# Optimization experiments

Measured on AMD Instinct MI355X. Metric: run time of the kernel, lower is better.

The kernel has to match this reference:

```python
import jax, jax.numpy as jnp
import numpy as np

B, N, D = 2, 2048, 1024
H, DH = 16, 64
DEPTH = 4
FF = 4
EPS = 1e-3  # keras LayerNormalization default epsilon
SCALE = DH ** -0.5


def setup_inputs() -> dict:
    key = jax.random.key(0)
    ks = jax.random.split(key, 8)
    s = 0.02
    inner = H * DH
    return {
        "x": jax.random.normal(ks[0], (B, N, D), jnp.float32),
        "mask": jnp.ones((B, N), jnp.bool_),
        "ln1_g": jnp.ones((DEPTH, D), jnp.float32),
        "ln1_b": jnp.zeros((DEPTH, D), jnp.float32),
        "Wqkv": jax.random.normal(ks[1], (DEPTH, D, 3 * inner), jnp.float32) * s,
        "Wout": jax.random.normal(ks[2], (DEPTH, inner, D), jnp.float32) * s,
        "bout": jnp.zeros((DEPTH, D), jnp.float32),
        "ln2_g": jnp.ones((DEPTH, D), jnp.float32),
        "ln2_b": jnp.zeros((DEPTH, D), jnp.float32),
        "W1": jax.random.normal(ks[3], (DEPTH, D, 2 * FF * D), jnp.float32) * s,
        "b1": jnp.zeros((DEPTH, 2 * FF * D), jnp.float32),
        "W2": jax.random.normal(ks[4], (DEPTH, FF * D, D), jnp.float32) * s,
        "b2": jnp.zeros((DEPTH, D), jnp.float32),
    }


def _layernorm(x, g, b):
    mu = jnp.mean(x, axis=-1, keepdims=True)
    var = jnp.mean(jnp.square(x - mu), axis=-1, keepdims=True)
    return (x - mu) * jax.lax.rsqrt(var + EPS) * g + b


def _attention(x, mask, Wqkv, Wout, bout):
    b, n, _ = x.shape
    qkv = x @ Wqkv  # [b, n, 3*h*dh]
    q, k, v = jnp.split(qkv, 3, axis=-1)
    split_heads = lambda t: t.reshape(b, n, H, DH).transpose(0, 2, 1, 3)  # b h n d
    q, k, v = split_heads(q), split_heads(k), split_heads(v)
    dots = jnp.einsum("bhid,bhjd->bhij", q, k) * SCALE
    neg = -jnp.finfo(dots.dtype).max
    # padding mask: keep (i valid) & (j valid)
    pm = mask[:, None, :, None] & mask[:, None, None, :]
    dots = jnp.where(pm, dots, neg)
    # causal mask: strict upper triangle masked out (triu with k=1)
    causal = jnp.triu(jnp.ones((n, n), jnp.bool_), k=1)
    dots = jnp.where(causal, neg, dots)
    attn = jax.nn.softmax(dots, axis=-1)
    out = jnp.einsum("bhij,bhjd->bhid", attn, v)
    out = out.transpose(0, 2, 1, 3).reshape(b, n, H * DH)
    return out @ Wout + bout


def _feedforward(x, W1, b1, W2, b2):
    h = x @ W1 + b1
    a, gates = jnp.split(h, 2, axis=-1)
    h = a * jax.nn.gelu(gates, approximate=False)  # GEGLU, tf.nn.gelu exact
    return h @ W2 + b2


def reference(x, mask, ln1_g, ln1_b, Wqkv, Wout, bout, ln2_g, ln2_b, W1, b1, W2, b2):
    for l in range(DEPTH):
        x = x + _attention(_layernorm(x, ln1_g[l], ln1_b[l]), mask, Wqkv[l], Wout[l], bout[l])
        x = x + _feedforward(_layernorm(x, ln2_g[l], ln2_b[l]), W1[l], b1[l], W2[l], b2[l])
    return x
```

## Files before the change

kernel.cpp:

```cpp
#include <hip/hip_runtime.h>


typedef float f32x4 __attribute__((ext_vector_type(4)));
typedef __bf16 bf16x8 __attribute__((ext_vector_type(8)));
typedef unsigned short u16;
typedef unsigned int u32;

#define SCALE2 0.18033688011112042f
#define LN_EPS 1e-3f
#define DEFER_THR 8.0f

__device__ __forceinline__ float fexp2(float x) { return __builtin_amdgcn_exp2f(x); }

__device__ __forceinline__ u16 f2bf(float f) {
  u32 u = __float_as_uint(f);
  u += 0x7fffu + ((u >> 16) & 1u);
  return (u16)(u >> 16);
}

__device__ __forceinline__ void stage16(void* lds_wave_base, const void* gsrc) {
  __builtin_amdgcn_global_load_lds((__attribute__((address_space(1))) void*)gsrc,
                                   (__attribute__((address_space(3))) void*)lds_wave_base,
                                   16, 0, 0);
}

__global__ void wtrans_kernel(const float* __restrict__ W, u16* __restrict__ WT,
                              int K, int N, int permMode) {
  __shared__ float tile[32][33];
  const int n0 = blockIdx.x * 32, k0 = blockIdx.y * 32;
  const float* Wl = W + (size_t)blockIdx.z * K * N;
  u16* WTl = WT + (size_t)blockIdx.z * K * N;
  const int tx = threadIdx.x, ty = threadIdx.y;
#pragma unroll
  for (int i = 0; i < 4; ++i)
    tile[ty + i * 8][tx] = Wl[(size_t)(k0 + ty + i * 8) * N + n0 + tx];
  __syncthreads();
#pragma unroll
  for (int i = 0; i < 4; ++i) {
    const int n = n0 + ty + i * 8;
    int orow;
    if (permMode) {
      orow = (n < 4096) ? (((n >> 4) << 5) + (n & 15))
                        : ((((n - 4096) >> 4) << 5) + 16 + (n & 15));
    } else {
      orow = n;
    }
    WTl[(size_t)orow * K + k0 + tx] = f2bf(tile[tx][ty + i * 8]);
  }
}

__global__ __launch_bounds__(256, 4)
void ln_kernel(const float* __restrict__ x, const float* __restrict__ g,
               const float* __restrict__ b, u16* __restrict__ y) {
  const int row = blockIdx.x, tid = threadIdx.x;
  const float4 v = ((const float4*)(x + (size_t)row * 1024))[tid];
  float s = v.x + v.y + v.z + v.w;
  float s2 = v.x * v.x + v.y * v.y + v.z * v.z + v.w * v.w;
#pragma unroll
  for (int off = 32; off > 0; off >>= 1) {
    s += __shfl_down(s, off);
    s2 += __shfl_down(s2, off);
  }
  __shared__ float ps[8];
  __shared__ float stats[2];
  const int wv = tid >> 6, lane = tid & 63;
  if (lane == 0) { ps[wv] = s; ps[wv + 4] = s2; }
  __syncthreads();
  if (tid == 0) {
    const float S = ps[0] + ps[1] + ps[2] + ps[3];
    const float S2 = ps[4] + ps[5] + ps[6] + ps[7];
    const float mu = S * (1.0f / 1024.0f);
    const float var = S2 * (1.0f / 1024.0f) - mu * mu;
    stats[0] = mu;
    stats[1] = rsqrtf(var + LN_EPS);
  }
  __syncthreads();
  const float mu = stats[0], rs = stats[1];
  const float4 gg = ((const float4*)g)[tid];
  const float4 bb = ((const float4*)b)[tid];
  ushort4 ov;
  ov.x = f2bf((v.x - mu) * rs * gg.x + bb.x);
  ov.y = f2bf((v.y - mu) * rs * gg.y + bb.y);
  ov.z = f2bf((v.z - mu) * rs * gg.z + bb.z);
  ov.w = f2bf((v.w - mu) * rs * gg.w + bb.w);
  ((ushort4*)(y + (size_t)row * 1024))[tid] = ov;
}

template <int EPI, int BM, int BN, int WM, int WN>
__global__ __launch_bounds__(WM * WN * 64, 2)
void gemm4(const u16* __restrict__ A, const u16* __restrict__ B,
           float* __restrict__ resid, const float* __restrict__ bias,
           u16* __restrict__ out, u16* __restrict__ vt, int M, int N, int K) {
  constexpr int NTHR = WM * WN * 64;
  constexpr int MT = BM / WM / 16;
  constexpr int NT = BN / WN / 16;
  __shared__ __align__(16) u16 lds[2][(BM + BN) * 64];

  const int tid = threadIdx.x;
  const int wv = tid >> 6, lane = tid & 63;
  const int lr = lane & 15, lg = lane >> 4;
  const int wmi = wv / WN, wni = wv % WN;
  const int RB0 = wmi * (BM / WM), CB0 = wni * (BN / WN);

  const int nwg = (int)(gridDim.x * gridDim.y);
  int id = (int)(blockIdx.y * gridDim.x + blockIdx.x);
  id = (id & 7) * (nwg >> 3) + (id >> 3);
  const int m0 = (id / (int)gridDim.x) * BM, n0 = (id % (int)gridDim.x) * BN;

  auto stage = [&](int bsel, int k0) {
    u16* dstA = &lds[bsel][0];
    u16* dstB = &lds[bsel][BM * 64];
#pragma unroll
    for (int rnd = 0; rnd < (BM * 128) / (NTHR * 16); ++rnd) {
      const int base = rnd * (NTHR * 16) + wv * 1024;
      const int off = base + lane * 16;
      const int row = off >> 7;
      const int k2 = (off & 127) ^ ((row & 7) << 4);
      stage16((char*)dstA + base, A + (size_t)(m0 + row) * K + k0 + (k2 >> 1));
    }
#pragma unroll
    for (int rnd = 0; rnd < (BN * 128) / (NTHR * 16); ++rnd) {
      const int base = rnd * (NTHR * 16) + wv * 1024;
      const int off = base + lane * 16;
      const int row = off >> 7;
      const int k2 = (off & 127) ^ ((row & 7) << 4);
      stage16((char*)dstB + base, B + (size_t)(n0 + row) * K + k0 + (k2 >> 1));
    }
  };

  f32x4 acc[MT][NT] = {};
  bf16x8 afr0[MT], bfr0[NT], afr1[MT], bfr1[NT];

  auto rd = [&](int bsel, int ks, bf16x8 (&af)[MT], bf16x8 (&bf)[NT]) {
    const char* As = (const char*)&lds[bsel][0];
    const char* Bs = (const char*)&lds[bsel][BM * 64];
#pragma unroll
    for (int mt = 0; mt < MT; ++mt) {
      const int row = RB0 + mt * 16 + lr;
      af[mt] = *(const bf16x8*)(As + row * 128 + ((ks * 64 + lg * 16) ^ ((lr & 7) << 4)));
    }
#pragma unroll
    for (int nt = 0; nt < NT; ++nt) {
      const int row = CB0 + nt * 16 + lr;
      bf[nt] = *(const bf16x8*)(Bs + row * 128 + ((ks * 64 + lg * 16) ^ ((lr & 7) << 4)));
    }
  };

  const int nT = K >> 6;
  stage(0, 0);
  stage(1, 64);
  asm volatile("s_waitcnt vmcnt(8)\n\ts_barrier" ::: "memory");
  rd(0, 0, afr0, bfr0);
  __builtin_amdgcn_sched_barrier(0);

  for (int t = 0; t < nT; ++t) {
    const int c = t & 1;
    rd(c, 1, afr1, bfr1);
    __builtin_amdgcn_sched_barrier(0);
    __builtin_amdgcn_s_setprio(1);
#pragma unroll
    for (int mt = 0; mt < MT; ++mt)
#pragma unroll
      for (int nt = 0; nt < NT; ++nt)
        acc[mt][nt] = __builtin_amdgcn_mfma_f32_16x16x32_bf16(
            afr0[mt], bfr0[nt], acc[mt][nt], 0, 0, 0);
    __builtin_amdgcn_s_setprio(0);
    __builtin_amdgcn_sched_barrier(0);
    asm volatile("s_waitcnt lgkmcnt(0)\n\ts_barrier" ::: "memory");
    __builtin_amdgcn_sched_barrier(0);
    if (t + 2 < nT) stage(c, (t + 2) * 64);
    if (t + 1 < nT) {
      if (t + 2 < nT)
        asm volatile("s_waitcnt vmcnt(8)\n\ts_barrier" ::: "memory");
      else
        asm volatile("s_waitcnt vmcnt(0)\n\ts_barrier" ::: "memory");
      rd(c ^ 1, 0, afr0, bfr0);
      __builtin_amdgcn_sched_barrier(0);
    }
    __builtin_amdgcn_s_setprio(1);
#pragma unroll
    for (int mt = 0; mt < MT; ++mt)
#pragma unroll
      for (int nt = 0; nt < NT; ++nt)
        acc[mt][nt] = __builtin_amdgcn_mfma_f32_16x16x32_bf16(
            afr1[mt], bfr1[nt], acc[mt][nt], 0, 0, 0);
    __builtin_amdgcn_s_setprio(0);
  }

  if (EPI == 0) {
#pragma unroll
    for (int mt = 0; mt < MT; ++mt)
#pragma unroll
      for (int nt = 0; nt < NT; ++nt) {
        const int n = n0 + CB0 + nt * 16 + lr;
#pragma unroll
        for (int r = 0; r < 4; ++r) {
          const int m = m0 + RB0 + mt * 16 + lg * 4 + r;
          out[(size_t)m * N + n] = f2bf(acc[mt][nt][r]);
        }
      }
  } else if (EPI == 1) {
    float bs[NT];
#pragma unroll
    for (int nt = 0; nt < NT; ++nt) bs[nt] = bias[n0 + CB0 + nt * 16 + lr];
#pragma unroll
    for (int mt = 0; mt < MT; ++mt)
#pragma unroll
      for (int nt = 0; nt < NT; ++nt) {
        const int n = n0 + CB0 + nt * 16 + lr;
#pragma unroll
        for (int r = 0; r < 4; ++r) {
          const int m = m0 + RB0 + mt * 16 + lg * 4 + r;
          resid[(size_t)m * N + n] += acc[mt][nt][r] + bs[nt];
        }
      }
  } else if (EPI == 2) {
#pragma unroll
    for (int pt = 0; pt < NT / 2; ++pt) {
      const int colA = ((n0 + CB0 + pt * 32) >> 5) * 16 + lr;
      const float ba = bias[colA];
      const float bg = bias[4096 + colA];
#pragma unroll
      for (int mt = 0; mt < MT; ++mt)
#pragma unroll
        for (int r = 0; r < 4; ++r) {
          const int m = m0 + RB0 + mt * 16 + lg * 4 + r;
          const float a = acc[mt][2 * pt][r] + ba;
          const float g = acc[mt][2 * pt + 1][r] + bg;
          const float gl = 0.5f * g * (1.0f + erff(g * 0.70710678118654752f));
          out[(size_t)m * 4096 + colA] = f2bf(a * gl);
        }
    }
  } else {
    if (n0 + CB0 < 2048) {
#pragma unroll
      for (int mt = 0; mt < MT; ++mt)
#pragma unroll
        for (int nt = 0; nt < NT; ++nt) {
          const int n = n0 + CB0 + nt * 16 + lr;
#pragma unroll
          for (int r = 0; r < 4; ++r) {
            const int m = m0 + RB0 + mt * 16 + lg * 4 + r;
            out[(size_t)m * N + n] = f2bf(acc[mt][nt][r]);
          }
        }
    } else {
      const int bidx = m0 >> 11;
      const int tokb = (m0 & 2047) + RB0 + lg * 4;
#pragma unroll
      for (int mt = 0; mt < MT; ++mt)
#pragma unroll
        for (int nt = 0; nt < NT; ++nt) {
          const int n = n0 + CB0 + nt * 16 + lr;
          const int hv = (n - 2048) >> 6;
          const int d = (n - 2048) & 63;
          ushort4 w;
          w.x = f2bf(acc[mt][nt][0]);
          w.y = f2bf(acc[mt][nt][1]);
          w.z = f2bf(acc[mt][nt][2]);
          w.w = f2bf(acc[mt][nt][3]);
          *(ushort4*)(vt + ((size_t)(bidx * 16 + hv) * 64 + d) * 2048 +
                      tokb + mt * 16) = w;
        }
    }
  }
}

__global__ __launch_bounds__(512, 4)
void attn_kernel(const u16* __restrict__ qkv, const u16* __restrict__ Vt,
                 u16* __restrict__ attnout) {
  __shared__ __align__(16) u16 KV[4][2][64 * 64];
  __shared__ __align__(16) u16 Ps[8][16 * 64];

  const int tid = threadIdx.x;
  const int wv = tid >> 6, lane = tid & 63;
  const int lr = lane & 15, lg = lane >> 4;
  const int lin = (int)(blockIdx.y * gridDim.x + blockIdx.x);
  const int xcd = lin & 7, j = lin >> 3;
  const int bh = xcd * 4 + (j >> 4);
  const int pr = j & 15;
  const int b = bh >> 4, h = bh & 15;
  const size_t tokbase = (size_t)b * 2048;
  const int qhi = 31 - pr;
  const int qt = (wv < 4) ? qhi : pr;
  const int ws = wv & 3;
  const int qg = qt * 64 + ws * 16 + lr;

  bf16x8 qf[2];
#pragma unroll
  for (int ks = 0; ks < 2; ++ks)
    qf[ks] = *(const bf16x8*)(qkv + (tokbase + qt * 64 + ws * 16 + lr) * 3072 +
                              h * 64 + ks * 32 + lg * 8);

  f32x4 o[4] = {};
  float m = -1e30f, lp = 0.f;

  const u16* kg_base = qkv + tokbase * 3072 + 1024 + h * 64;
  const u16* vg_base = Vt + (size_t)bh * 64 * 2048;

  const int soff = tid * 16;
  const int srow = soff >> 7;
  const int scol = (soff & 127) ^ ((srow & 7) << 4);
  auto stage = [&](int bsel, int kt2) {
    stage16((char*)&KV[bsel][0][0] + wv * 1024,
            kg_base + (size_t)(kt2 * 64 + srow) * 3072 + (scol >> 1));
    stage16((char*)&KV[bsel][1][0] + wv * 1024,
            vg_base + (size_t)srow * 2048 + kt2 * 64 + (scol >> 1));
  };

  auto compute = [&](int kt) {
    const char* Ks = (const char*)&KV[kt & 3][0][0];
    const char* Vs = (const char*)&KV[kt & 3][1][0];

    f32x4 s[4] = {};
#pragma unroll
    for (int ks = 0; ks < 2; ++ks)
#pragma unroll
      for (int nt = 0; nt < 4; ++nt) {
        const int row = nt * 16 + lr;
        const bf16x8 kf = *(const bf16x8*)(Ks + row * 128 +
                                           ((ks * 64 + lg * 16) ^ ((lr & 7) << 4)));
        s[nt] = __builtin_amdgcn_mfma_f32_16x16x32_bf16(kf, qf[ks], s[nt], 0, 0, 0);
      }

    float pmax = -1e30f;
    const bool diag = (kt == qt);
#pragma unroll
    for (int nt = 0; nt < 4; ++nt)
#pragma unroll
      for (int r = 0; r < 4; ++r) {
        float v = s[nt][r] * SCALE2;
        if (diag) {
          const int kg = kt * 64 + nt * 16 + lg * 4 + r;
          v = (kg <= qg) ? v : -1e30f;
        }
        s[nt][r] = v;
        pmax = fmaxf(pmax, v);
      }

    if (!__all(pmax - m <= DEFER_THR)) {
      float mx = fmaxf(pmax, __shfl_xor(pmax, 16));
      mx = fmaxf(mx, __shfl_xor(mx, 32));
      const float mn = fmaxf(m, mx);
      const float alpha = fexp2(m - mn);
      m = mn;
      lp *= alpha;
#pragma unroll
      for (int r = 0; r < 4; ++r) {
        const float ar = __shfl(alpha, lg * 4 + r);
#pragma unroll
        for (int dt = 0; dt < 4; ++dt) o[dt][r] *= ar;
      }
    }

#pragma unroll
    for (int nt = 0; nt < 4; ++nt) {
      const float p0 = fexp2(s[nt][0] - m), p1 = fexp2(s[nt][1] - m);
      const float p2 = fexp2(s[nt][2] - m), p3 = fexp2(s[nt][3] - m);
      lp += (p0 + p1) + (p2 + p3);
      uint2 w;
      w.x = (u32)f2bf(p0) | ((u32)f2bf(p1) << 16);
      w.y = (u32)f2bf(p2) | ((u32)f2bf(p3) << 16);
      *(uint2*)((char*)&Ps[wv][0] + lr * 128 + ((nt * 32 + lg * 8) ^ ((lr & 7) << 4))) = w;
    }

    bf16x8 pf[2];
#pragma unroll
    for (int ks = 0; ks < 2; ++ks) {
      const int jp = (ks * 4 + lg) ^ (lr & 7);
      pf[ks] = *(const bf16x8*)(&Ps[wv][0] + lr * 64 + jp * 8);
    }
#pragma unroll
    for (int ks = 0; ks < 2; ++ks)
#pragma unroll
      for (int dt = 0; dt < 4; ++dt) {
        const int row = dt * 16 + lr;
        const bf16x8 vf = *(const bf16x8*)(Vs + row * 128 +
                                           ((ks * 64 + lg * 16) ^ ((lr & 7) << 4)));
        o[dt] = __builtin_amdgcn_mfma_f32_16x16x32_bf16(pf[ks], vf, o[dt], 0, 0, 0);
      }
  };

  stage(0, 0); stage(1, 1); stage(2, 2); stage(3, 3);
  asm volatile("s_waitcnt vmcnt(4)\n\ts_barrier" ::: "memory");

  for (int kt = 0; kt <= qhi; kt += 2) {
    if (kt <= qt) compute(kt);
    if (kt + 1 <= qt) compute(kt + 1);
    asm volatile("s_barrier" ::: "memory");
    if (kt + 4 <= qhi) stage((kt + 4) & 3, kt + 4);
    if (kt + 5 <= qhi) stage((kt + 5) & 3, kt + 5);
    if (kt + 2 <= qhi) {
      if (kt + 4 <= qhi)
        asm volatile("s_waitcnt vmcnt(4)\n\ts_barrier" ::: "memory");
      else
        asm volatile("s_waitcnt vmcnt(0)\n\ts_barrier" ::: "memory");
    }
  }

  float lsum = lp + __shfl_xor(lp, 16);
  lsum += __shfl_xor(lsum, 32);
#pragma unroll
  for (int r = 0; r < 4; ++r) {
    const float ld = __shfl(lsum, lg * 4 + r);
    const int tok = qt * 64 + ws * 16 + lg * 4 + r;
#pragma unroll
    for (int dt = 0; dt < 4; ++dt)
      attnout[(tokbase + tok) * 1024 + h * 64 + dt * 16 + lr] = f2bf(o[dt][r] / ld);
  }
}

extern "C" void kernel_launch(void* const* d_in, const int* in_sizes, int n_in,
                              void* d_out, int out_size, void* d_ws, size_t ws_size,
                              hipStream_t stream) {
  (void)in_sizes; (void)n_in; (void)ws_size;
  const float* x_in  = (const float*)d_in[0];
  const float* ln1_g = (const float*)d_in[2];
  const float* ln1_b = (const float*)d_in[3];
  const float* Wqkv  = (const float*)d_in[4];
  const float* Wout  = (const float*)d_in[5];
  const float* bout  = (const float*)d_in[6];
  const float* ln2_g = (const float*)d_in[7];
  const float* ln2_b = (const float*)d_in[8];
  const float* W1    = (const float*)d_in[9];
  const float* b1    = (const float*)d_in[10];
  const float* W2    = (const float*)d_in[11];
  const float* b2    = (const float*)d_in[12];
  float* x = (float*)d_out;

  char* ws = (char*)d_ws;
  size_t off = 0;
  auto alloc = [&](size_t bytes) -> void* {
    void* p = ws + off;
    off += (bytes + 255) & ~(size_t)255;
    return p;
  };
  u16* WqkvT = (u16*)alloc(4ull * 3072 * 1024 * 2);
  u16* WoutT = (u16*)alloc(4ull * 1024 * 1024 * 2);
  u16* W1T   = (u16*)alloc(4ull * 8192 * 1024 * 2);
  u16* W2T   = (u16*)alloc(4ull * 1024 * 4096 * 2);
  u16* y     = (u16*)alloc(4096ull * 1024 * 2);
  u16* qkvb  = (u16*)alloc(4096ull * 3072 * 2);
  u16* Vt    = (u16*)alloc(32ull * 64 * 2048 * 2);
  u16* attn  = (u16*)alloc(4096ull * 1024 * 2);
  u16* ff    = (u16*)alloc(4096ull * 4096 * 2);

  hipMemcpyAsync(x, x_in, (size_t)out_size * 4, hipMemcpyDeviceToDevice, stream);

  const dim3 tb(32, 8);
  wtrans_kernel<<<dim3(3072 / 32, 1024 / 32, 4), tb, 0, stream>>>(Wqkv, WqkvT, 1024, 3072, 0);
  wtrans_kernel<<<dim3(1024 / 32, 1024 / 32, 4), tb, 0, stream>>>(Wout, WoutT, 1024, 1024, 0);
  wtrans_kernel<<<dim3(8192 / 32, 1024 / 32, 4), tb, 0, stream>>>(W1, W1T, 1024, 8192, 1);
  wtrans_kernel<<<dim3(1024 / 32, 4096 / 32, 4), tb, 0, stream>>>(W2, W2T, 4096, 1024, 0);

  for (int l = 0; l < 4; ++l) {
    ln_kernel<<<4096, 256, 0, stream>>>(x, ln1_g + l * 1024, ln1_b + l * 1024, y);
    gemm4<3, 128, 128, 2, 2><<<dim3(3072 / 128, 4096 / 128), 256, 0, stream>>>(
        y, WqkvT + (size_t)l * 3072 * 1024, nullptr, nullptr, qkvb, Vt, 4096, 3072, 1024);
    attn_kernel<<<dim3(16, 32), 512, 0, stream>>>(qkvb, Vt, attn);
    gemm4<1, 128, 128, 2, 2><<<dim3(1024 / 128, 4096 / 128), 256, 0, stream>>>(
        attn, WoutT + (size_t)l * 1024 * 1024, x, bout + l * 1024, nullptr, nullptr,
        4096, 1024, 1024);
    ln_kernel<<<4096, 256, 0, stream>>>(x, ln2_g + l * 1024, ln2_b + l * 1024, y);
    gemm4<2, 256, 256, 2, 4><<<dim3(8192 / 256, 4096 / 256), 512, 0, stream>>>(
        y, W1T + (size_t)l * 8192 * 1024, nullptr, b1 + l * 8192, ff, nullptr,
        4096, 8192, 1024);
    gemm4<1, 128, 128, 2, 2><<<dim3(1024 / 128, 4096 / 128), 256, 0, stream>>>(
        ff, W2T + (size_t)l * 1024 * 4096, x, b2 + l * 1024, nullptr, nullptr,
        4096, 1024, 4096);
  }
}
```

Before: 1.118 ms.

## Replace GEMM template with fixed 128x128 tile, K-step 32 kernel

Replaces the templated GEMM with a fixed 128x128, 4-wave kernel that stages K in 32-wide chunks with a new XOR swizzle, and drops the register double-buffering of LDS fragments. LDS use per block shrinks, so launch bounds rise to 4 blocks per CU for higher occupancy. The FF1 GEMM moves from 256x256 tiles to 128x128 tiles. The trade-off is more barriers per K, less latency hiding from fragment prefetch, and lower reuse for the large GEMM.

After: 1.239 ms. 1.11x slower.

```diff
diff --git a/kernel.cpp b/kernel.cpp
--- a/kernel.cpp
+++ b/kernel.cpp
@@ -86,112 +86,91 @@
   ((ushort4*)(y + (size_t)row * 1024))[tid] = ov;
 }
 
-template <int EPI, int BM, int BN, int WM, int WN>
-__global__ __launch_bounds__(WM * WN * 64, 2)
-void gemm4(const u16* __restrict__ A, const u16* __restrict__ B,
+template <int EPI>
+__global__ __launch_bounds__(256, 4)
+void gemm6(const u16* __restrict__ A, const u16* __restrict__ B,
            float* __restrict__ resid, const float* __restrict__ bias,
            u16* __restrict__ out, u16* __restrict__ vt, int M, int N, int K) {
-  constexpr int NTHR = WM * WN * 64;
-  constexpr int MT = BM / WM / 16;
-  constexpr int NT = BN / WN / 16;
-  __shared__ __align__(16) u16 lds[2][(BM + BN) * 64];
+  __shared__ __align__(16) u16 lds[2][256 * 32];
 
   const int tid = threadIdx.x;
   const int wv = tid >> 6, lane = tid & 63;
   const int lr = lane & 15, lg = lane >> 4;
-  const int wmi = wv / WN, wni = wv % WN;
-  const int RB0 = wmi * (BM / WM), CB0 = wni * (BN / WN);
+  const int wmi = wv >> 1, wni = wv & 1;
+  const int RB0 = wmi * 64, CB0 = wni * 64;
 
   const int nwg = (int)(gridDim.x * gridDim.y);
   int id = (int)(blockIdx.y * gridDim.x + blockIdx.x);
   id = (id & 7) * (nwg >> 3) + (id >> 3);
-  const int m0 = (id / (int)gridDim.x) * BM, n0 = (id % (int)gridDim.x) * BN;
+  const int m0 = (id / (int)gridDim.x) * 128, n0 = (id % (int)gridDim.x) * 128;
 
   auto stage = [&](int bsel, int k0) {
     u16* dstA = &lds[bsel][0];
-    u16* dstB = &lds[bsel][BM * 64];
-#pragma unroll
-    for (int rnd = 0; rnd < (BM * 128) / (NTHR * 16); ++rnd) {
-      const int base = rnd * (NTHR * 16) + wv * 1024;
+    u16* dstB = &lds[bsel][128 * 32];
+#pragma unroll
+    for (int rnd = 0; rnd < 2; ++rnd) {
+      const int base = rnd * 4096 + wv * 1024;
       const int off = base + lane * 16;
-      const int row = off >> 7;
-      const int k2 = (off & 127) ^ ((row & 7) << 4);
-      stage16((char*)dstA + base, A + (size_t)(m0 + row) * K + k0 + (k2 >> 1));
-    }
-#pragma unroll
-    for (int rnd = 0; rnd < (BN * 128) / (NTHR * 16); ++rnd) {
-      const int base = rnd * (NTHR * 16) + wv * 1024;
+      const int row = off >> 6;
+      const int gslot = ((off >> 4) & 3) ^ ((row >> 1) & 3);
+      stage16((char*)dstA + base, A + (size_t)(m0 + row) * K + k0 + gslot * 8);
+    }
+#pragma unroll
+    for (int rnd = 0; rnd < 2; ++rnd) {
+      const int base = rnd * 4096 + wv * 1024;
       const int off = base + lane * 16;
-      const int row = off >> 7;
-      const int k2 = (off & 127) ^ ((row & 7) << 4);
-      stage16((char*)dstB + base, B + (size_t)(n0 + row) * K + k0 + (k2 >> 1));
+      const int row = off >> 6;
+      const int gslot = ((off >> 4) & 3) ^ ((row >> 1) & 3);
+      stage16((char*)dstB + base, B + (size_t)(n0 + row) * K + k0 + gslot * 8);
     }
   };
 
-  f32x4 acc[MT][NT] = {};
-  bf16x8 afr0[MT], bfr0[NT], afr1[MT], bfr1[NT];
-
-  auto rd = [&](int bsel, int ks, bf16x8 (&af)[MT], bf16x8 (&bf)[NT]) {
-    const char* As = (const char*)&lds[bsel][0];
-    const char* Bs = (const char*)&lds[bsel][BM * 64];
-#pragma unroll
-    for (int mt = 0; mt < MT; ++mt) {
-      const int row = RB0 + mt * 16 + lr;
-      af[mt] = *(const bf16x8*)(As + row * 128 + ((ks * 64 + lg * 16) ^ ((lr & 7) << 4)));
-    }
-#pragma unroll
-    for (int nt = 0; nt < NT; ++nt) {
-      const int row = CB0 + nt * 16 + lr;
-      bf[nt] = *(const bf16x8*)(Bs + row * 128 + ((ks * 64 + lg * 16) ^ ((lr & 7) << 4)));
-    }
-  };
-
-  const int nT = K >> 6;
+  f32x4 acc[4][4] = {};
+  bf16x8 af[4], bf[4];
+
+  const int nT = K >> 5;
   stage(0, 0);
-  stage(1, 64);
-  asm volatile("s_waitcnt vmcnt(8)\n\ts_barrier" ::: "memory");
-  rd(0, 0, afr0, bfr0);
-  __builtin_amdgcn_sched_barrier(0);
+  stage(1, 32);
+  asm volatile("s_waitcnt vmcnt(4)\n\ts_barrier" ::: "memory");
 
   for (int t = 0; t < nT; ++t) {
     const int c = t & 1;
-    rd(c, 1, afr1, bfr1);
-    __builtin_amdgcn_sched_barrier(0);
+    const char* As = (const char*)&lds[c][0];
+    const char* Bs = (const char*)&lds[c][128 * 32];
+#pragma unroll
+    for (int mt = 0; mt < 4; ++mt) {
+      const int row = RB0 + mt * 16 + lr;
+      af[mt] = *(const bf16x8*)(As + row * 64 + ((lg * 16) ^ (((row >> 1) & 3) << 4)));
+    }
+#pragma unroll
+    for (int nt = 0; nt < 4; ++nt) {
+      const int row = CB0 + nt * 16 + lr;
+      bf[nt] = *(const bf16x8*)(Bs + row * 64 + ((lg * 16) ^ (((row >> 1) & 3) << 4)));
+    }
     __builtin_amdgcn_s_setprio(1);
 #pragma unroll
-    for (int mt = 0; mt < MT; ++mt)
-#pragma unroll
-      for (int nt = 0; nt < NT; ++nt)
+    for (int mt = 0; mt < 4; ++mt)
+#pragma unroll
+      for (int nt = 0; nt < 4; ++nt)
         acc[mt][nt] = __builtin_amdgcn_mfma_f32_16x16x32_bf16(
-            afr0[mt], bfr0[nt], acc[mt][nt], 0, 0, 0);
+            af[mt], bf[nt], acc[mt][nt], 0, 0, 0);
     __builtin_amdgcn_s_setprio(0);
-    __builtin_amdgcn_sched_barrier(0);
     asm volatile("s_waitcnt lgkmcnt(0)\n\ts_barrier" ::: "memory");
     __builtin_amdgcn_sched_barrier(0);
-    if (t + 2 < nT) stage(c, (t + 2) * 64);
+    if (t + 2 < nT) stage(c, (t + 2) * 32);
     if (t + 1 < nT) {
       if (t + 2 < nT)
-        asm volatile("s_waitcnt vmcnt(8)\n\ts_barrier" ::: "memory");
+        asm volatile("s_waitcnt vmcnt(4)\n\ts_barrier" ::: "memory");
       else
         asm volatile("s_waitcnt vmcnt(0)\n\ts_barrier" ::: "memory");
-      rd(c ^ 1, 0, afr0, bfr0);
-      __builtin_amdgcn_sched_barrier(0);
-    }
-    __builtin_amdgcn_s_setprio(1);
-#pragma unroll
-    for (int mt = 0; mt < MT; ++mt)
-#pragma unroll
-      for (int nt = 0; nt < NT; ++nt)
-        acc[mt][nt] = __builtin_amdgcn_mfma_f32_16x16x32_bf16(
-            afr1[mt], bfr1[nt], acc[mt][nt], 0, 0, 0);
-    __builtin_amdgcn_s_setprio(0);
+    }
   }
 
   if (EPI == 0) {
 #pragma unroll
-    for (int mt = 0; mt < MT; ++mt)
-#pragma unroll
-      for (int nt = 0; nt < NT; ++nt) {
+    for (int mt = 0; mt < 4; ++mt)
+#pragma unroll
+      for (int nt = 0; nt < 4; ++nt) {
         const int n = n0 + CB0 + nt * 16 + lr;
 #pragma unroll
         for (int r = 0; r < 4; ++r) {
@@ -200,13 +179,13 @@
         }
       }
   } else if (EPI == 1) {
-    float bs[NT];
-#pragma unroll
-    for (int nt = 0; nt < NT; ++nt) bs[nt] = bias[n0 + CB0 + nt * 16 + lr];
-#pragma unroll
-    for (int mt = 0; mt < MT; ++mt)
-#pragma unroll
-      for (int nt = 0; nt < NT; ++nt) {
+    float bs[4];
+#pragma unroll
+    for (int nt = 0; nt < 4; ++nt) bs[nt] = bias[n0 + CB0 + nt * 16 + lr];
+#pragma unroll
+    for (int mt = 0; mt < 4; ++mt)
+#pragma unroll
+      for (int nt = 0; nt < 4; ++nt) {
         const int n = n0 + CB0 + nt * 16 + lr;
 #pragma unroll
         for (int r = 0; r < 4; ++r) {
@@ -216,12 +195,12 @@
       }
   } else if (EPI == 2) {
 #pragma unroll
-    for (int pt = 0; pt < NT / 2; ++pt) {
+    for (int pt = 0; pt < 2; ++pt) {
       const int colA = ((n0 + CB0 + pt * 32) >> 5) * 16 + lr;
       const float ba = bias[colA];
       const float bg = bias[4096 + colA];
 #pragma unroll
-      for (int mt = 0; mt < MT; ++mt)
+      for (int mt = 0; mt < 4; ++mt)
 #pragma unroll
         for (int r = 0; r < 4; ++r) {
           const int m = m0 + RB0 + mt * 16 + lg * 4 + r;
@@ -234,9 +213,9 @@
   } else {
     if (n0 + CB0 < 2048) {
 #pragma unroll
-      for (int mt = 0; mt < MT; ++mt)
-#pragma unroll
-        for (int nt = 0; nt < NT; ++nt) {
+      for (int mt = 0; mt < 4; ++mt)
+#pragma unroll
+        for (int nt = 0; nt < 4; ++nt) {
           const int n = n0 + CB0 + nt * 16 + lr;
 #pragma unroll
           for (int r = 0; r < 4; ++r) {
@@ -248,9 +227,9 @@
       const int bidx = m0 >> 11;
       const int tokb = (m0 & 2047) + RB0 + lg * 4;
 #pragma unroll
-      for (int mt = 0; mt < MT; ++mt)
-#pragma unroll
-        for (int nt = 0; nt < NT; ++nt) {
+      for (int mt = 0; mt < 4; ++mt)
+#pragma unroll
+        for (int nt = 0; nt < 4; ++nt) {
           const int n = n0 + CB0 + nt * 16 + lr;
           const int hv = (n - 2048) >> 6;
           const int d = (n - 2048) & 63;
@@ -455,17 +434,17 @@
 
   for (int l = 0; l < 4; ++l) {
     ln_kernel<<<4096, 256, 0, stream>>>(x, ln1_g + l * 1024, ln1_b + l * 1024, y);
-    gemm4<3, 128, 128, 2, 2><<<dim3(3072 / 128, 4096 / 128), 256, 0, stream>>>(
+    gemm6<3><<<dim3(3072 / 128, 4096 / 128), 256, 0, stream>>>(
         y, WqkvT + (size_t)l * 3072 * 1024, nullptr, nullptr, qkvb, Vt, 4096, 3072, 1024);
     attn_kernel<<<dim3(16, 32), 512, 0, stream>>>(qkvb, Vt, attn);
-    gemm4<1, 128, 128, 2, 2><<<dim3(1024 / 128, 4096 / 128), 256, 0, stream>>>(
+    gemm6<1><<<dim3(1024 / 128, 4096 / 128), 256, 0, stream>>>(
         attn, WoutT + (size_t)l * 1024 * 1024, x, bout + l * 1024, nullptr, nullptr,
         4096, 1024, 1024);
     ln_kernel<<<4096, 256, 0, stream>>>(x, ln2_g + l * 1024, ln2_b + l * 1024, y);
-    gemm4<2, 256, 256, 2, 4><<<dim3(8192 / 256, 4096 / 256), 512, 0, stream>>>(
+    gemm6<2><<<dim3(8192 / 128, 4096 / 128), 256, 0, stream>>>(
         y, W1T + (size_t)l * 8192 * 1024, nullptr, b1 + l * 8192, ff, nullptr,
         4096, 8192, 1024);
-    gemm4<1, 128, 128, 2, 2><<<dim3(1024 / 128, 4096 / 128), 256, 0, stream>>>(
+    gemm6<1><<<dim3(1024 / 128, 4096 / 128), 256, 0, stream>>>(
         ff, W2T + (size_t)l * 1024 * 4096, x, b2 + l * 1024, nullptr, nullptr,
         4096, 1024, 4096);
   }
```
